# Kernel optimization log

Hardware: AMD Instinct MI355X
Metric: run time of the kernel (lower is better)

The kernel has to match this reference:

```python
import jax, jax.numpy as jnp
import numpy as np

B, S, D, H, DFF = 2, 2048, 1024, 16, 4096
HD = D // H
EPS = 1e-5


def setup_inputs() -> dict:
    key = jax.random.key(0)
    ks = jax.random.split(key, 8)
    s = lambda fan_in: 1.0 / np.sqrt(fan_in)
    return {
        "x": jax.random.normal(ks[0], (B, S, D), jnp.float32),
        "ln1_g": jnp.ones((D,), jnp.float32),
        "ln1_b": jnp.zeros((D,), jnp.float32),
        "Wq": jax.random.normal(ks[1], (D, D), jnp.float32) * s(D),
        "Wk": jax.random.normal(ks[2], (D, D), jnp.float32) * s(D),
        "Wv": jax.random.normal(ks[3], (D, D), jnp.float32) * s(D),
        "Wo": jax.random.normal(ks[4], (D, D), jnp.float32) * s(D),
        "bo": jnp.zeros((D,), jnp.float32),
        "ln2_g": jnp.ones((D,), jnp.float32),
        "ln2_b": jnp.zeros((D,), jnp.float32),
        "W1": jax.random.normal(ks[5], (D, DFF), jnp.float32) * s(D),
        "b1": jnp.zeros((DFF,), jnp.float32),
        "W2": jax.random.normal(ks[6], (DFF, D), jnp.float32) * s(DFF),
        "b2": jnp.zeros((D,), jnp.float32),
    }


def _layernorm(x, g, b):
    mu = jnp.mean(x, axis=-1, keepdims=True)
    var = jnp.var(x, axis=-1, keepdims=True)
    return (x - mu) * jax.lax.rsqrt(var + EPS) * g + b


def reference(x, ln1_g, ln1_b, Wq, Wk, Wv, Wo, bo, ln2_g, ln2_b, W1, b1, W2, b2):
    # --- pre-LN + causal multi-head attention + residual ---
    h = _layernorm(x, ln1_g, ln1_b)
    q = (h @ Wq).reshape(B, S, H, HD).transpose(0, 2, 1, 3)  # [B,H,S,hd]
    k = (h @ Wk).reshape(B, S, H, HD).transpose(0, 2, 1, 3)
    v = (h @ Wv).reshape(B, S, H, HD).transpose(0, 2, 1, 3)
    scores = jnp.einsum("bhqd,bhkd->bhqk", q, k) / jnp.sqrt(jnp.float32(HD))
    causal = jnp.triu(jnp.ones((S, S), bool), k=1)  # True above diagonal -> masked
    scores = jnp.where(causal, -jnp.inf, scores)
    attn = jax.nn.softmax(scores, axis=-1)  # dropout is identity at inference
    ctx = jnp.einsum("bhqk,bhkd->bhqd", attn, v)
    ctx = ctx.transpose(0, 2, 1, 3).reshape(B, S, D)
    x = x + ctx @ Wo + bo
    # --- pre-LN + MLP + residual ---
    h = _layernorm(x, ln2_g, ln2_b)
    h = jax.nn.gelu(h @ W1 + b1, approximate=False)  # torch nn.GELU default = exact
    x = x + h @ W2 + b2
    return x
```

## Files before the change

### kernel.cpp

```cpp
#include <hip/hip_runtime.h>
#include <hip/hip_bf16.h>
#include <math.h>

using bf16 = __hip_bfloat16;
typedef short bf16x8 __attribute__((ext_vector_type(8)));
typedef float f32x4 __attribute__((ext_vector_type(4)));

static constexpr int B = 2, S = 2048, D = 1024, H = 16, HD = 64, DFF = 4096;
static constexpr int NR = B * S;
static constexpr int DQ = 3072;
static constexpr float EPS = 1e-5f;

__device__ __forceinline__ bf16 f2b(float v) { return __float2bfloat16(v); }

__device__ __forceinline__ float gelu_exact(float v) {
    const float u = v * 0.70710678118654752f;
    const float au = fabsf(u);
    const float t = __builtin_amdgcn_rcpf(1.0f + 0.3275911f * au);
    float poly = 1.061405429f;
    poly = poly * t - 1.453152027f;
    poly = poly * t + 1.421413741f;
    poly = poly * t - 0.284496736f;
    poly = poly * t + 0.254829592f;
    poly = poly * t;
    const float ea = 1.0f - poly * __expf(-u * u);
    return 0.5f * v * (1.0f + copysignf(ea, u));
}

typedef __attribute__((address_space(1))) const void* gp1_t;
typedef __attribute__((address_space(3))) void* sp3_t;
__device__ __forceinline__ void gld_lds16(const bf16* g, bf16* l) {
    __builtin_amdgcn_global_load_lds((gp1_t)(const void*)g, (sp3_t)(void*)l, 16, 0, 0);
}

__device__ __forceinline__ void convT_body(const float* __restrict__ src,
                                           bf16* __restrict__ dst,
                                           int K, int N, int k0, int n0, int tid) {
    __shared__ float tile[64][65];
    const int r = tid >> 4, c = (tid & 15) * 4;
#pragma unroll
    for (int rr = 0; rr < 64; rr += 16) {
        float4 v = *(const float4*)&src[(size_t)(k0 + r + rr) * N + n0 + c];
        tile[r + rr][c] = v.x; tile[r + rr][c + 1] = v.y;
        tile[r + rr][c + 2] = v.z; tile[r + rr][c + 3] = v.w;
    }
    __syncthreads();
    const int n = tid >> 2, ks = (tid & 3) * 16;
    union { bf16 h[16]; int4 v2[2]; } o;
#pragma unroll
    for (int i = 0; i < 16; ++i) o.h[i] = f2b(tile[ks + i][n]);
    bf16* dp = &dst[(size_t)(n0 + n) * K + k0 + ks];
    *(int4*)dp = o.v2[0];
    *(int4*)(dp + 8) = o.v2[1];
}

__global__ __launch_bounds__(256) void convT_kernel(const float* __restrict__ src,
                                                    bf16* __restrict__ dst,
                                                    int K, int N) {
    convT_body(src, dst, K, N, blockIdx.x * 64, blockIdx.y * 64, threadIdx.x);
}

__device__ __forceinline__ void ln_body(const float* __restrict__ x,
                                        const float* __restrict__ g,
                                        const float* __restrict__ b,
                                        bf16* __restrict__ out, int row, int tid) {
    const float4 v4 = ((const float4*)(x + (size_t)row * D))[tid];
    float v[4] = {v4.x, v4.y, v4.z, v4.w};
    float s = v[0] + v[1] + v[2] + v[3];
    float sq = v[0] * v[0] + v[1] * v[1] + v[2] * v[2] + v[3] * v[3];
#pragma unroll
    for (int off = 32; off >= 1; off >>= 1) {
        s += __shfl_xor(s, off);
        sq += __shfl_xor(sq, off);
    }
    __shared__ float ssum[4], ssq[4];
    const int wave = tid >> 6;
    if ((tid & 63) == 0) { ssum[wave] = s; ssq[wave] = sq; }
    __syncthreads();
    s = ssum[0] + ssum[1] + ssum[2] + ssum[3];
    sq = ssq[0] + ssq[1] + ssq[2] + ssq[3];
    const float mu = s * (1.0f / D);
    const float var = sq * (1.0f / D) - mu * mu;
    const float rstd = rsqrtf(var + EPS);
    bf16* orow = out + (size_t)row * D;
#pragma unroll
    for (int i = 0; i < 4; ++i) {
        const int c = tid * 4 + i;
        orow[c] = f2b((v[i] - mu) * rstd * g[c] + b[c]);
    }
}

__global__ __launch_bounds__(256) void ln_kernel(const float* __restrict__ x,
                                                 const float* __restrict__ g,
                                                 const float* __restrict__ b,
                                                 bf16* __restrict__ out) {
    ln_body(x, g, b, out, blockIdx.x, threadIdx.x);
}

__global__ __launch_bounds__(256) void prep_kernel(const float* __restrict__ Wq,
                                                   const float* __restrict__ Wk,
                                                   const float* __restrict__ Wv,
                                                   const float* __restrict__ Wo,
                                                   const float* __restrict__ W2,
                                                   const float* __restrict__ W1,
                                                   bf16* __restrict__ WqkvT,
                                                   bf16* __restrict__ WoT,
                                                   bf16* __restrict__ W2T,
                                                   bf16* __restrict__ W1T,
                                                   const float* __restrict__ x,
                                                   const float* __restrict__ ln1_g,
                                                   const float* __restrict__ ln1_b,
                                                   bf16* __restrict__ h,
                                                   int nW) {
    const int bid = blockIdx.x;
    const int tid = threadIdx.x;
    if (bid >= nW) { ln_body(x, ln1_g, ln1_b, h, bid - nW, tid); return; }
    const float* src;
    bf16* dst;
    int K, N, bx, by;
    if (bid < 768) {
        const int j = bid >> 8, r = bid & 255;
        src = (j == 0) ? Wq : ((j == 1) ? Wk : Wv);
        dst = WqkvT + (size_t)j * D * D;
        K = D; N = D; bx = r & 15; by = r >> 4;
    } else if (bid < 1024) {
        const int r = bid - 768;
        src = Wo; dst = WoT; K = D; N = D; bx = r & 15; by = r >> 4;
    } else if (bid < 2048) {
        const int r = bid - 1024;
        src = W2; dst = W2T; K = DFF; N = D; bx = r & 63; by = r >> 6;
    } else {
        const int r = bid - 2048;
        src = W1; dst = W1T; K = D; N = DFF; bx = r & 15; by = r >> 4;
    }
    convT_body(src, dst, K, N, bx * 64, by * 64, tid);
}

template <int EPI, int BN>
__global__ __launch_bounds__(256) void gemm_bt(const bf16* __restrict__ A,
                                               const bf16* __restrict__ Bt,
                                               const float* __restrict__ bias,
                                               const float* __restrict__ res,
                                               void* __restrict__ Cv,
                                               int M, int N, int K) {
    constexpr int NTW = BN / 32;
    constexpr int AHALF = 128 * 32;
    constexpr int BHALF = BN * 32;
    constexpr int ASZ = 2 * AHALF, BSZ = 2 * BHALF;
    constexpr int CST = BN + 8;
    __shared__ __align__(16) bf16 smem[2 * (ASZ + BSZ)];

    const int Mtiles = M / 128;
    const int p = blockIdx.x;
    const int tm = p % Mtiles;
    const int tn = p / Mtiles;
    const int tid = threadIdx.x;
    const int wave = tid >> 6, lane = tid & 63;
    const int wm = wave >> 1, wn = wave & 1;
    const int quad = lane >> 4, l16 = lane & 15;

    const int r4 = tid >> 2, s4 = (tid & 3) * 8;
    const size_t K64 = (size_t)64 * K;
    const int nk = K / 64;

    f32x4 acc[4][NTW];
#pragma unroll
    for (int i = 0; i < 4; ++i)
#pragma unroll
        for (int j = 0; j < NTW; ++j) acc[i][j] = (f32x4){0.f, 0.f, 0.f, 0.f};

    const bf16* Ap = A + (size_t)(tm * 128 + r4) * K + s4;
    const bf16* Bp = Bt + (size_t)(tn * BN + r4) * K + s4;

    gld_lds16(Ap, smem + tid * 8);
    gld_lds16(Ap + K64, smem + (256 + tid) * 8);
    gld_lds16(Ap + 32, smem + (512 + tid) * 8);
    gld_lds16(Ap + K64 + 32, smem + (768 + tid) * 8);
    gld_lds16(Bp, smem + 2 * ASZ + tid * 8);
    gld_lds16(Bp + 32, smem + 2 * ASZ + (256 + tid) * 8);
    Ap += 64;
    Bp += 64;

    float rv[4][NTW][4];

    for (int kt = 0; kt < nk; ++kt) {
        const int cur = kt & 1, nxt = cur ^ 1;
        bf16* Acur = smem + cur * ASZ;
        bf16* Bcur = smem + 2 * ASZ + cur * BSZ;
        __syncthreads();
        if (kt + 1 < nk) {
            bf16* Anxt = smem + nxt * ASZ;
            bf16* Bnxt = smem + 2 * ASZ + nxt * BSZ;
            gld_lds16(Ap, Anxt + tid * 8);
            gld_lds16(Ap + K64, Anxt + (256 + tid) * 8);
            gld_lds16(Ap + 32, Anxt + (512 + tid) * 8);
            gld_lds16(Ap + K64 + 32, Anxt + (768 + tid) * 8);
            gld_lds16(Bp, Bnxt + tid * 8);
            gld_lds16(Bp + 32, Bnxt + (256 + tid) * 8);
            Ap += 64;
            Bp += 64;
        }

        if constexpr (EPI == 1) {
            if (kt == nk - 2) {
#pragma unroll
                for (int nt = 0; nt < NTW; ++nt) {
                    const int col = tn * BN + wn * (BN / 2) + nt * 16 + l16;
#pragma unroll
                    for (int mt = 0; mt < 4; ++mt) {
                        const int row0 = tm * 128 + wm * 64 + mt * 16 + quad * 4;
#pragma unroll
                        for (int j = 0; j < 4; ++j)
                            rv[mt][nt][j] = res[(size_t)(row0 + j) * N + col];
                    }
                }
            }
        }

#pragma unroll
        for (int ks = 0; ks < 2; ++ks) {
            const bf16* Ah = Acur + ks * AHALF;
            const bf16* Bh = Bcur + ks * BHALF;
            bf16x8 aF[4], bF[NTW];
#pragma unroll
            for (int mt = 0; mt < 4; ++mt)
                aF[mt] = *(const bf16x8*)(Ah + (wm * 64 + mt * 16 + l16) * 32 + quad * 8);
#pragma unroll
            for (int nt = 0; nt < NTW; ++nt)
                bF[nt] = *(const bf16x8*)(Bh + (wn * (BN / 2) + nt * 16 + l16) * 32 + quad * 8);
#pragma unroll
            for (int mt = 0; mt < 4; ++mt)
#pragma unroll
                for (int nt = 0; nt < NTW; ++nt)
                    acc[mt][nt] = __builtin_amdgcn_mfma_f32_16x16x32_bf16(
                        aF[mt], bF[nt], acc[mt][nt], 0, 0, 0);
        }
    }

    if constexpr (EPI == 1) {
#pragma unroll
        for (int nt = 0; nt < NTW; ++nt) {
            const int col = tn * BN + wn * (BN / 2) + nt * 16 + l16;
            const float bv = bias[col];
#pragma unroll
            for (int mt = 0; mt < 4; ++mt) {
                const int row0 = tm * 128 + wm * 64 + mt * 16 + quad * 4;
#pragma unroll
                for (int j = 0; j < 4; ++j) {
                    const size_t idx = (size_t)(row0 + j) * N + col;
                    ((float*)Cv)[idx] = acc[mt][nt][j] + bv + rv[mt][nt][j];
                }
            }
        }
    } else {
        bf16* C = (bf16*)Cv;
        __syncthreads();
#pragma unroll
        for (int nt = 0; nt < NTW; ++nt) {
            const int ccol = wn * (BN / 2) + nt * 16 + l16;
            float bv = 0.f;
            if (EPI == 2) bv = bias[tn * BN + ccol];
#pragma unroll
            for (int mt = 0; mt < 4; ++mt) {
                const int r0 = wm * 64 + mt * 16 + quad * 4;
#pragma unroll
                for (int j = 0; j < 4; ++j) {
                    float v = acc[mt][nt][j];
                    if (EPI == 2) v = gelu_exact(v + bv);
                    smem[(r0 + j) * CST + ccol] = f2b(v);
                }
            }
        }
        __syncthreads();
        bf16* crow = C + (size_t)(tm * 128) * N + tn * BN;
#pragma unroll
        for (int i = 0; i < BN / 16; ++i) {
            const int gid = i * 256 + tid;
            const int row = gid / (BN / 8), c8 = gid % (BN / 8);
            const int4 val = *(const int4*)(smem + row * CST + c8 * 8);
            *(int4*)(crow + (size_t)row * N + c8 * 8) = val;
        }
    }
}

__global__ __launch_bounds__(256) void fattn_kernel(const bf16* __restrict__ QKV,
                                                    bf16* __restrict__ ctx) {
    const int id = blockIdx.x;
    const int bh = id & 31;
    const int k = id >> 5;
    const int t = (k < 16) ? 31 - k : k - 16;
    const int b = bh >> 4, h = bh & (H - 1);
    const int tid = threadIdx.x;
    const int wave = tid >> 6, lane = tid & 63;
    const int quad = lane >> 4, l16 = lane & 15;
    const bf16* Qp = QKV + (size_t)b * S * DQ + h * HD;
    const bf16* Kp = Qp + D;
    const bf16* Vp = Qp + 2 * D;

    __shared__ __align__(16) bf16 Ks[2][64 * 64];
    __shared__ __align__(16) bf16 Vt[2][64][72];

    const int keyA = tid >> 3;
    const int sA = (keyA & 3) | ((keyA >> 1) & 4);
    const int dsA = ((tid & 7) ^ sA) * 8;
    const size_t K32 = (size_t)32 * DQ;

    const int q0 = t * 64;
    const bf16* qg = Qp + (size_t)(q0 + wave * 16 + l16) * DQ + quad * 8;
    union U8 { bf16 h[8]; bf16x8 v; };
    U8 uq0, uq1;
    uq0.v = *(const bf16x8*)(qg);
    uq1.v = *(const bf16x8*)(qg + 32);
#pragma unroll
    for (int i = 0; i < 8; ++i) {
        uq0.h[i] = f2b(__bfloat162float(uq0.h[i]) * 0.125f);
        uq1.h[i] = f2b(__bfloat162float(uq1.h[i]) * 0.125f);
    }
    const bf16x8 aQ0 = uq0.v;
    const bf16x8 aQ1 = uq1.v;

    const int kb = (l16 >> 2) * 8 + (l16 & 3);
    const int sQ = (l16 & 3) | (((l16 >> 2) & 1) << 2);
    const int ofs0 = kb * 64 + ((quad ^ sQ) * 8);
    const int ofs1 = kb * 64 + (((4 + quad) ^ sQ) * 8);

    f32x4 O[4];
#pragma unroll
    for (int nt = 0; nt < 4; ++nt) O[nt] = (f32x4){0.f, 0.f, 0.f, 0.f};
    float rowm = -3.0e38f, rowl = 0.f;

    gld_lds16(Kp + (size_t)keyA * DQ + dsA, Ks[0] + tid * 8);
    gld_lds16(Kp + K32 + (size_t)keyA * DQ + dsA, Ks[0] + (256 + tid) * 8);
    {
        const bf16* vg = Vp + (size_t)lane * DQ + wave * 16;
        U8 u0, u1;
        u0.v = *(const bf16x8*)vg;
        u1.v = *(const bf16x8*)(vg + 8);
#pragma unroll
        for (int i = 0; i < 8; ++i) {
            Vt[0][wave * 16 + i][lane] = u0.h[i];
            Vt[0][wave * 16 + 8 + i][lane] = u1.h[i];
        }
    }

    const int nch = t + 1;
    for (int c = 0; c < nch; ++c) {
        const int cur = c & 1, nxt = cur ^ 1;
        __syncthreads();
        U8 u0, u1;
        if (c + 1 < nch) {
            const bf16* kg = Kp + (size_t)((c + 1) * 64 + keyA) * DQ + dsA;
            gld_lds16(kg, Ks[nxt] + tid * 8);
            gld_lds16(kg + K32, Ks[nxt] + (256 + tid) * 8);
            const bf16* vg = Vp + (size_t)((c + 1) * 64 + lane) * DQ + wave * 16;
            u0.v = *(const bf16x8*)vg;
            u1.v = *(const bf16x8*)(vg + 8);
        }

        f32x4 sc[4];
        __builtin_amdgcn_s_setprio(1);
#pragma unroll
        for (int m = 0; m < 4; ++m) {
            const bf16* kr = Ks[cur] + (m & 1) * 256 + (m >> 1) * 2048;
            const bf16x8 bK0 = *(const bf16x8*)(kr + ofs0);
            const bf16x8 bK1 = *(const bf16x8*)(kr + ofs1);
            f32x4 z = (f32x4){0.f, 0.f, 0.f, 0.f};
            z = __builtin_amdgcn_mfma_f32_16x16x32_bf16(bK0, aQ0, z, 0, 0, 0);
            z = __builtin_amdgcn_mfma_f32_16x16x32_bf16(bK1, aQ1, z, 0, 0, 0);
            sc[m] = z;
        }
        __builtin_amdgcn_s_setprio(0);
        if (c == nch - 1) {
            const int qloc = wave * 16 + l16;
#pragma unroll
            for (int m = 0; m < 4; ++m) {
                const int kk = quad * 8 + (m & 1) * 4 + (m >> 1) * 32;
#pragma unroll
                for (int j = 0; j < 4; ++j)
                    if (kk + j > qloc) sc[m][j] = -3.0e38f;
            }
        }
        f32x4 mv;
#pragma unroll
        for (int j = 0; j < 4; ++j)
            mv[j] = fmaxf(fmaxf(sc[0][j], sc[1][j]), fmaxf(sc[2][j], sc[3][j]));
        float mx = fmaxf(fmaxf(mv[0], mv[1]), fmaxf(mv[2], mv[3]));
        mx = fmaxf(mx, __shfl_xor(mx, 16));
        mx = fmaxf(mx, __shfl_xor(mx, 32));
        if (__any(mx > rowm + 8.0f)) {
            const float mn = fmaxf(rowm, mx);
            const float alq = __expf(rowm - mn);
            rowm = mn;
            rowl *= alq;
#pragma unroll
            for (int nt = 0; nt < 4; ++nt)
#pragma unroll
                for (int j = 0; j < 4; ++j) O[nt][j] *= alq;
        }
        float rs = 0.f;
#pragma unroll
        for (int m = 0; m < 4; ++m)
#pragma unroll
            for (int j = 0; j < 4; ++j) {
                sc[m][j] = __expf(sc[m][j] - rowm);
                rs += sc[m][j];
            }
        rs += __shfl_xor(rs, 16);
        rs += __shfl_xor(rs, 32);
        rowl += rs;

        U8 p0, p1;
#pragma unroll
        for (int j = 0; j < 4; ++j) {
            p0.h[j]     = f2b(sc[0][j]);
            p0.h[4 + j] = f2b(sc[1][j]);
            p1.h[j]     = f2b(sc[2][j]);
            p1.h[4 + j] = f2b(sc[3][j]);
        }
        __builtin_amdgcn_s_setprio(1);
#pragma unroll
        for (int nt = 0; nt < 4; ++nt) {
            const bf16x8 bV0 = *(const bf16x8*)&Vt[cur][nt * 16 + l16][quad * 8];
            const bf16x8 bV1 = *(const bf16x8*)&Vt[cur][nt * 16 + l16][32 + quad * 8];
            O[nt] = __builtin_amdgcn_mfma_f32_16x16x32_bf16(bV0, p0.v, O[nt], 0, 0, 0);
            O[nt] = __builtin_amdgcn_mfma_f32_16x16x32_bf16(bV1, p1.v, O[nt], 0, 0, 0);
        }
        __builtin_amdgcn_s_setprio(0);
        if (c + 1 < nch) {
#pragma unroll
            for (int i = 0; i < 8; ++i) {
                Vt[nxt][wave * 16 + i][lane] = u0.h[i];
                Vt[nxt][wave * 16 + 8 + i][lane] = u1.h[i];
            }
        }
    }

    const float rlq = 1.0f / rowl;
    bf16* crow = ctx + (size_t)b * S * D + h * HD + (size_t)(q0 + wave * 16 + l16) * D;
#pragma unroll
    for (int nt = 0; nt < 4; ++nt) {
        union { bf16 h[4]; int2 v; } o;
#pragma unroll
        for (int j = 0; j < 4; ++j) o.h[j] = f2b(O[nt][j] * rlq);
        *(int2*)(crow + nt * 16 + quad * 4) = o.v;
    }
}

extern "C" void kernel_launch(void* const* d_in, const int* in_sizes, int n_in,
                              void* d_out, int out_size, void* d_ws, size_t ws_size,
                              hipStream_t stream) {
    const float* x     = (const float*)d_in[0];
    const float* ln1_g = (const float*)d_in[1];
    const float* ln1_b = (const float*)d_in[2];
    const float* Wq    = (const float*)d_in[3];
    const float* Wk    = (const float*)d_in[4];
    const float* Wv    = (const float*)d_in[5];
    const float* Wo    = (const float*)d_in[6];
    const float* bo    = (const float*)d_in[7];
    const float* ln2_g = (const float*)d_in[8];
    const float* ln2_b = (const float*)d_in[9];
    const float* W1    = (const float*)d_in[10];
    const float* b1    = (const float*)d_in[11];
    const float* W2    = (const float*)d_in[12];
    const float* b2    = (const float*)d_in[13];
    float* out = (float*)d_out;

    char* ws = (char*)d_ws;
    const size_t MB = (size_t)1 << 20;
    const bool wide = ws_size >= 72 * MB;
    bf16* h     = (bf16*)(ws + 0 * MB);
    bf16* QKVb  = (bf16*)(ws + 8 * MB);
    bf16* hff   = (bf16*)(ws + 8 * MB);
    bf16* ctx   = (bf16*)(ws + 32 * MB);
    bf16* h2    = (bf16*)(ws + 40 * MB);
    bf16* WqkvT = (bf16*)(ws + 48 * MB);
    bf16* WoT   = (bf16*)(ws + 54 * MB);
    bf16* W2T   = (bf16*)(ws + 56 * MB);
    bf16* W1T   = wide ? (bf16*)(ws + 64 * MB) : (bf16*)(ws + 0 * MB);

    const int nW = wide ? 3072 : 2048;
    prep_kernel<<<nW + NR, 256, 0, stream>>>(
        Wq, Wk, Wv, Wo, W2, W1, WqkvT, WoT, W2T, W1T, x, ln1_g, ln1_b, h, nW);
    gemm_bt<0, 64><<<(NR / 128) * (DQ / 64), 256, 0, stream>>>(
        h, WqkvT, nullptr, nullptr, QKVb, NR, DQ, D);
    if (!wide) convT_kernel<<<dim3(16, 64), 256, 0, stream>>>(W1, W1T, D, DFF);
    fattn_kernel<<<dim3((S / 64) * B * H), 256, 0, stream>>>(QKVb, ctx);
    gemm_bt<1, 64><<<(NR / 128) * (D / 64), 256, 0, stream>>>(
        ctx, WoT, bo, x, out, NR, D, D);
    ln_kernel<<<NR, 256, 0, stream>>>(out, ln2_g, ln2_b, h2);
    gemm_bt<2, 64><<<(NR / 128) * (DFF / 64), 256, 0, stream>>>(
        h2, W1T, b1, nullptr, hff, NR, DFF, D);
    gemm_bt<1, 64><<<(NR / 128) * (D / 64), 256, 0, stream>>>(
        hff, W2T, b2, out, out, NR, D, DFF);
}
```

Measured before the change: 319.0 us.

## Process 128 query rows per attention block with two 16-row groups per wave

The flash attention kernel now gives each block a 128-row query tile instead of 64, with each wave handling two 16-row groups that share the same K and V tiles staged in LDS. This halves the number of blocks and the total K/V global-to-LDS traffic, and doubles the MFMA work per LDS load. The cost is more registers per thread (two sets of O accumulators and softmax state), fewer blocks for load balancing across CUs, and more masked work on the diagonal chunks.

```diff
diff --git a/kernel.cpp b/kernel.cpp
--- a/kernel.cpp
+++ b/kernel.cpp
@@ -288,7 +288,7 @@
     const int id = blockIdx.x;
     const int bh = id & 31;
     const int k = id >> 5;
-    const int t = (k < 16) ? 31 - k : k - 16;
+    const int t = (k < 8) ? 15 - k : k - 8;
     const int b = bh >> 4, h = bh & (H - 1);
     const int tid = threadIdx.x;
     const int wave = tid >> 6, lane = tid & 63;
@@ -305,29 +305,32 @@
     const int dsA = ((tid & 7) ^ sA) * 8;
     const size_t K32 = (size_t)32 * DQ;
 
-    const int q0 = t * 64;
-    const bf16* qg = Qp + (size_t)(q0 + wave * 16 + l16) * DQ + quad * 8;
+    const int q0 = t * 128;
     union U8 { bf16 h[8]; bf16x8 v; };
-    U8 uq0, uq1;
-    uq0.v = *(const bf16x8*)(qg);
-    uq1.v = *(const bf16x8*)(qg + 32);
-#pragma unroll
-    for (int i = 0; i < 8; ++i) {
-        uq0.h[i] = f2b(__bfloat162float(uq0.h[i]) * 0.125f);
-        uq1.h[i] = f2b(__bfloat162float(uq1.h[i]) * 0.125f);
-    }
-    const bf16x8 aQ0 = uq0.v;
-    const bf16x8 aQ1 = uq1.v;
+    U8 uq[2][2];
+#pragma unroll
+    for (int g = 0; g < 2; ++g) {
+        const bf16* qg = Qp + (size_t)(q0 + wave * 32 + g * 16 + l16) * DQ + quad * 8;
+        uq[g][0].v = *(const bf16x8*)(qg);
+        uq[g][1].v = *(const bf16x8*)(qg + 32);
+#pragma unroll
+        for (int i = 0; i < 8; ++i) {
+            uq[g][0].h[i] = f2b(__bfloat162float(uq[g][0].h[i]) * 0.125f);
+            uq[g][1].h[i] = f2b(__bfloat162float(uq[g][1].h[i]) * 0.125f);
+        }
+    }
 
     const int kb = (l16 >> 2) * 8 + (l16 & 3);
     const int sQ = (l16 & 3) | (((l16 >> 2) & 1) << 2);
     const int ofs0 = kb * 64 + ((quad ^ sQ) * 8);
     const int ofs1 = kb * 64 + (((4 + quad) ^ sQ) * 8);
 
-    f32x4 O[4];
-#pragma unroll
-    for (int nt = 0; nt < 4; ++nt) O[nt] = (f32x4){0.f, 0.f, 0.f, 0.f};
-    float rowm = -3.0e38f, rowl = 0.f;
+    f32x4 O[2][4];
+#pragma unroll
+    for (int g = 0; g < 2; ++g)
+#pragma unroll
+        for (int nt = 0; nt < 4; ++nt) O[g][nt] = (f32x4){0.f, 0.f, 0.f, 0.f};
+    float rowm[2] = {-3.0e38f, -3.0e38f}, rowl[2] = {0.f, 0.f};
 
     gld_lds16(Kp + (size_t)keyA * DQ + dsA, Ks[0] + tid * 8);
     gld_lds16(Kp + K32 + (size_t)keyA * DQ + dsA, Ks[0] + (256 + tid) * 8);
@@ -343,7 +346,7 @@
         }
     }
 
-    const int nch = t + 1;
+    const int nch = 2 * t + 2;
     for (int c = 0; c < nch; ++c) {
         const int cur = c & 1, nxt = cur ^ 1;
         __syncthreads();
@@ -357,73 +360,86 @@
             u1.v = *(const bf16x8*)(vg + 8);
         }
 
-        f32x4 sc[4];
+        f32x4 sc[2][4];
         __builtin_amdgcn_s_setprio(1);
 #pragma unroll
         for (int m = 0; m < 4; ++m) {
             const bf16* kr = Ks[cur] + (m & 1) * 256 + (m >> 1) * 2048;
             const bf16x8 bK0 = *(const bf16x8*)(kr + ofs0);
             const bf16x8 bK1 = *(const bf16x8*)(kr + ofs1);
-            f32x4 z = (f32x4){0.f, 0.f, 0.f, 0.f};
-            z = __builtin_amdgcn_mfma_f32_16x16x32_bf16(bK0, aQ0, z, 0, 0, 0);
-            z = __builtin_amdgcn_mfma_f32_16x16x32_bf16(bK1, aQ1, z, 0, 0, 0);
-            sc[m] = z;
+#pragma unroll
+            for (int g = 0; g < 2; ++g) {
+                f32x4 z = (f32x4){0.f, 0.f, 0.f, 0.f};
+                z = __builtin_amdgcn_mfma_f32_16x16x32_bf16(bK0, uq[g][0].v, z, 0, 0, 0);
+                z = __builtin_amdgcn_mfma_f32_16x16x32_bf16(bK1, uq[g][1].v, z, 0, 0, 0);
+                sc[g][m] = z;
+            }
         }
         __builtin_amdgcn_s_setprio(0);
-        if (c == nch - 1) {
-            const int qloc = wave * 16 + l16;
-#pragma unroll
-            for (int m = 0; m < 4; ++m) {
-                const int kk = quad * 8 + (m & 1) * 4 + (m >> 1) * 32;
-#pragma unroll
-                for (int j = 0; j < 4; ++j)
-                    if (kk + j > qloc) sc[m][j] = -3.0e38f;
-            }
-        }
-        f32x4 mv;
-#pragma unroll
-        for (int j = 0; j < 4; ++j)
-            mv[j] = fmaxf(fmaxf(sc[0][j], sc[1][j]), fmaxf(sc[2][j], sc[3][j]));
-        float mx = fmaxf(fmaxf(mv[0], mv[1]), fmaxf(mv[2], mv[3]));
-        mx = fmaxf(mx, __shfl_xor(mx, 16));
-        mx = fmaxf(mx, __shfl_xor(mx, 32));
-        if (__any(mx > rowm + 8.0f)) {
-            const float mn = fmaxf(rowm, mx);
-            const float alq = __expf(rowm - mn);
-            rowm = mn;
-            rowl *= alq;
-#pragma unroll
-            for (int nt = 0; nt < 4; ++nt)
-#pragma unroll
-                for (int j = 0; j < 4; ++j) O[nt][j] *= alq;
-        }
-        float rs = 0.f;
-#pragma unroll
-        for (int m = 0; m < 4; ++m)
+        if (c >= 2 * t) {
+            const int kb0 = (c - 2 * t) * 64;
+#pragma unroll
+            for (int g = 0; g < 2; ++g) {
+                const int qloc = wave * 32 + g * 16 + l16;
+#pragma unroll
+                for (int m = 0; m < 4; ++m) {
+                    const int kk = kb0 + quad * 8 + (m & 1) * 4 + (m >> 1) * 32;
+#pragma unroll
+                    for (int j = 0; j < 4; ++j)
+                        if (kk + j > qloc) sc[g][m][j] = -3.0e38f;
+                }
+            }
+        }
+        U8 p[2][2];
+#pragma unroll
+        for (int g = 0; g < 2; ++g) {
+            f32x4 mv;
+#pragma unroll
+            for (int j = 0; j < 4; ++j)
+                mv[j] = fmaxf(fmaxf(sc[g][0][j], sc[g][1][j]),
+                              fmaxf(sc[g][2][j], sc[g][3][j]));
+            float mx = fmaxf(fmaxf(mv[0], mv[1]), fmaxf(mv[2], mv[3]));
+            mx = fmaxf(mx, __shfl_xor(mx, 16));
+            mx = fmaxf(mx, __shfl_xor(mx, 32));
+            if (__any(mx > rowm[g] + 8.0f)) {
+                const float mn = fmaxf(rowm[g], mx);
+                const float alq = __expf(rowm[g] - mn);
+                rowm[g] = mn;
+                rowl[g] *= alq;
+#pragma unroll
+                for (int nt = 0; nt < 4; ++nt)
+#pragma unroll
+                    for (int j = 0; j < 4; ++j) O[g][nt][j] *= alq;
+            }
+            float rs = 0.f;
+#pragma unroll
+            for (int m = 0; m < 4; ++m)
+#pragma unroll
+                for (int j = 0; j < 4; ++j) {
+                    sc[g][m][j] = __expf(sc[g][m][j] - rowm[g]);
+                    rs += sc[g][m][j];
+                }
+            rs += __shfl_xor(rs, 16);
+            rs += __shfl_xor(rs, 32);
+            rowl[g] += rs;
 #pragma unroll
             for (int j = 0; j < 4; ++j) {
-                sc[m][j] = __expf(sc[m][j] - rowm);
-                rs += sc[m][j];
-            }
-        rs += __shfl_xor(rs, 16);
-        rs += __shfl_xor(rs, 32);
-        rowl += rs;
-
-        U8 p0, p1;
-#pragma unroll
-        for (int j = 0; j < 4; ++j) {
-            p0.h[j]     = f2b(sc[0][j]);
-            p0.h[4 + j] = f2b(sc[1][j]);
-            p1.h[j]     = f2b(sc[2][j]);
-            p1.h[4 + j] = f2b(sc[3][j]);
+                p[g][0].h[j]     = f2b(sc[g][0][j]);
+                p[g][0].h[4 + j] = f2b(sc[g][1][j]);
+                p[g][1].h[j]     = f2b(sc[g][2][j]);
+                p[g][1].h[4 + j] = f2b(sc[g][3][j]);
+            }
         }
         __builtin_amdgcn_s_setprio(1);
 #pragma unroll
         for (int nt = 0; nt < 4; ++nt) {
             const bf16x8 bV0 = *(const bf16x8*)&Vt[cur][nt * 16 + l16][quad * 8];
             const bf16x8 bV1 = *(const bf16x8*)&Vt[cur][nt * 16 + l16][32 + quad * 8];
-            O[nt] = __builtin_amdgcn_mfma_f32_16x16x32_bf16(bV0, p0.v, O[nt], 0, 0, 0);
-            O[nt] = __builtin_amdgcn_mfma_f32_16x16x32_bf16(bV1, p1.v, O[nt], 0, 0, 0);
+#pragma unroll
+            for (int g = 0; g < 2; ++g) {
+                O[g][nt] = __builtin_amdgcn_mfma_f32_16x16x32_bf16(bV0, p[g][0].v, O[g][nt], 0, 0, 0);
+                O[g][nt] = __builtin_amdgcn_mfma_f32_16x16x32_bf16(bV1, p[g][1].v, O[g][nt], 0, 0, 0);
+            }
         }
         __builtin_amdgcn_s_setprio(0);
         if (c + 1 < nch) {
@@ -435,14 +451,18 @@
         }
     }
 
-    const float rlq = 1.0f / rowl;
-    bf16* crow = ctx + (size_t)b * S * D + h * HD + (size_t)(q0 + wave * 16 + l16) * D;
-#pragma unroll
-    for (int nt = 0; nt < 4; ++nt) {
-        union { bf16 h[4]; int2 v; } o;
-#pragma unroll
-        for (int j = 0; j < 4; ++j) o.h[j] = f2b(O[nt][j] * rlq);
-        *(int2*)(crow + nt * 16 + quad * 4) = o.v;
+#pragma unroll
+    for (int g = 0; g < 2; ++g) {
+        const float rlq = 1.0f / rowl[g];
+        bf16* crow = ctx + (size_t)b * S * D + h * HD +
+                     (size_t)(q0 + wave * 32 + g * 16 + l16) * D;
+#pragma unroll
+        for (int nt = 0; nt < 4; ++nt) {
+            union { bf16 h[4]; int2 v; } o;
+#pragma unroll
+            for (int j = 0; j < 4; ++j) o.h[j] = f2b(O[g][nt][j] * rlq);
+            *(int2*)(crow + nt * 16 + quad * 4) = o.v;
+        }
     }
 }
 
@@ -484,7 +504,7 @@
     gemm_bt<0, 64><<<(NR / 128) * (DQ / 64), 256, 0, stream>>>(
         h, WqkvT, nullptr, nullptr, QKVb, NR, DQ, D);
     if (!wide) convT_kernel<<<dim3(16, 64), 256, 0, stream>>>(W1, W1T, D, DFF);
-    fattn_kernel<<<dim3((S / 64) * B * H), 256, 0, stream>>>(QKVb, ctx);
+    fattn_kernel<<<dim3((S / 128) * B * H), 256, 0, stream>>>(QKVb, ctx);
     gemm_bt<1, 64><<<(NR / 128) * (D / 64), 256, 0, stream>>>(
         ctx, WoT, bo, x, out, NR, D, D);
     ln_kernel<<<NR, 256, 0, stream>>>(out, ln2_g, ln2_b, h2);
```

New measurement: 332.1 us. 4.1% more time.
